# Optimization experiments

Measured on AMD Instinct MI355X. Metric: run time of the kernel, lower is better.

## Reference

```python
import jax, jax.numpy as jnp
import numpy as np

N_NODES = 100000
N_EDGES = 1600000
IN_CH = 128
HID = 128
OUT_CH = 64
N_GRAPHS = 512


def gcn_conv(x, edge_index, W, b):
    # GCNConv (PyG defaults): add self-loops, symmetric normalization
    # out = D^{-1/2} (A + I) D^{-1/2} X W + b
    n = x.shape[0]
    loop = jnp.arange(n, dtype=edge_index.dtype)
    src = jnp.concatenate([edge_index[0], loop])
    dst = jnp.concatenate([edge_index[1], loop])
    deg = jax.ops.segment_sum(jnp.ones_like(dst, x.dtype), dst, num_segments=n)
    dinv = jnp.where(deg > 0, jax.lax.rsqrt(deg), jnp.zeros_like(deg))
    norm = dinv[src] * dinv[dst]            # [E+N]
    h = x @ W                                # [N, out] transform first (dense GEMM)
    msg = h[src] * norm[:, None]             # gather + scale  [E+N, out]
    return jax.ops.segment_sum(msg, dst, num_segments=n) + b


def global_mean_pool(x, batch, num_graphs):
    sums = jax.ops.segment_sum(x, batch, num_segments=num_graphs)
    cnts = jax.ops.segment_sum(jnp.ones_like(batch, x.dtype), batch, num_segments=num_graphs)
    return sums / jnp.maximum(cnts, 1.0)[:, None]


def setup_inputs() -> dict:
    key = jax.random.key(0)
    ks = jax.random.split(key, 12)
    x = jax.random.normal(ks[0], (N_NODES, IN_CH), dtype=jnp.float32)
    edge_index = jax.random.randint(ks[1], (2, N_EDGES), 0, N_NODES, dtype=jnp.int64)
    batch = jnp.sort(jax.random.randint(ks[2], (N_NODES,), 0, N_GRAPHS, dtype=jnp.int64))
    def glorot(k, fi, fo):
        s = float(np.sqrt(6.0 / (fi + fo)))
        return jax.random.uniform(k, (fi, fo), jnp.float32, -s, s)
    W1 = glorot(ks[3], IN_CH, HID); b1 = jnp.zeros((HID,), jnp.float32)
    W2 = glorot(ks[4], HID, HID);   b2 = jnp.zeros((HID,), jnp.float32)
    W3 = glorot(ks[5], HID, HID);   b3 = jnp.zeros((HID,), jnp.float32)
    W4 = glorot(ks[6], HID, OUT_CH); b4 = jnp.zeros((OUT_CH,), jnp.float32)
    return {"x": x, "edge_index": edge_index, "batch": batch,
            "W1": W1, "b1": b1, "W2": W2, "b2": b2,
            "W3": W3, "b3": b3, "W4": W4, "b4": b4}


def reference(x, edge_index, batch, W1, b1, W2, b2, W3, b3, W4, b4):
    h = jax.nn.relu(gcn_conv(x, edge_index, W1, b1))
    h = jax.nn.relu(gcn_conv(h, edge_index, W2, b2))
    g = global_mean_pool(h, batch, N_GRAPHS)           # [G, HID]
    # MLP head; Dropout(0.2) is identity in eval mode
    g = jax.nn.relu(g @ W3 + b3)
    return g @ W4 + b4                                  # [G, OUT_CH]
```

## Files before the change

kernel.cpp:

```cpp
#include <hip/hip_runtime.h>

#define NN 100000
#define EE 1600000
#define CH 128
#define NG 512
#define OC 64

#define CSH 10
#define NCB 98
#define PBLK 256
#define PCHUNK 6250
#define SCAP 128

#define O_DINV   0
#define O_ROWS   100032
#define O_CNT    200064
#define O_PART   225152
#define O_OFFS   225280
#define O_START  225408
#define O_CSR    225984
#define O_HS     2726016
#define O_STG    9126080
#define O_WT1    9126080
#define O_WT2    9142464
#define O_A1     14800448

typedef __attribute__((ext_vector_type(8))) short short8v;
typedef __attribute__((ext_vector_type(4))) float float4v;

static __device__ __forceinline__ unsigned short f2bf(float x) {
  unsigned u = __float_as_uint(x);
  return (unsigned short)((u + 0x7FFFu + ((u >> 16) & 1u)) >> 16);
}
static __device__ __forceinline__ float bf2f(unsigned short h) {
  return __uint_as_float((unsigned)h << 16);
}
static __device__ __forceinline__ unsigned pack2(float a, float b) {
  return (unsigned)f2bf(a) | ((unsigned)f2bf(b) << 16);
}
static __device__ __forceinline__ float bflo(unsigned v) {
  return __uint_as_float(v << 16);
}
static __device__ __forceinline__ float bfhi(unsigned v) {
  return __uint_as_float(v & 0xFFFF0000u);
}

__global__ __launch_bounds__(1024) void k_part(const int* __restrict__ src,
                                               const int* __restrict__ dst,
                                               int* __restrict__ cnt,
                                               unsigned* __restrict__ stg) {
  __shared__ int hist[NCB];
  __shared__ int lcur[NCB];
  __shared__ unsigned lout[PCHUNK];
  int t = threadIdx.x;
  int e0 = blockIdx.x * PCHUNK;
  if (t < NCB) { hist[t] = 0; lcur[t] = 0; }
  __syncthreads();
  for (int e = e0 + t; e < e0 + PCHUNK; e += 1024)
    atomicAdd(&hist[dst[e] >> CSH], 1);
  __syncthreads();
  if (t == 0) {
    int s = 0;
    for (int i = 0; i < NCB; ++i) { int v = hist[i]; hist[i] = s; s += v; }
  }
  __syncthreads();
  for (int e = e0 + t; e < e0 + PCHUNK; e += 1024) {
    int d = dst[e];
    int b = d >> CSH;
    int p = hist[b] + atomicAdd(&lcur[b], 1);
    lout[p] = (unsigned)src[e] | ((unsigned)(d & 1023) << 17);
  }
  __syncthreads();
  int w = t >> 6, lane = t & 63;
  unsigned* mystg = stg + (size_t)blockIdx.x * NCB * SCAP;
  for (int b = w; b < NCB; b += 16) {
    int beg = hist[b];
    int end = (b == NCB - 1) ? PCHUNK : hist[b + 1];
    int n = min(end - beg, SCAP);
    for (int i = lane; i < n; i += 64) mystg[b * SCAP + i] = lout[beg + i];
    if (lane == 0) cnt[blockIdx.x * NCB + b] = n;
  }
}

__global__ __launch_bounds__(1024) void k_count(const unsigned* __restrict__ stg,
                                                const int* __restrict__ cnt,
                                                int* __restrict__ rows,
                                                int* __restrict__ part,
                                                float* __restrict__ dinv) {
  __shared__ int ldeg[1024];
  __shared__ int s[1024];
  int b = blockIdx.x;
  int t = threadIdx.x;
  int w = t >> 6, lane = t & 63;
  int gid = (b << CSH) + t;
  ldeg[t] = 0;
  __syncthreads();
  for (int blk = w; blk < PBLK; blk += 16) {
    int c = cnt[blk * NCB + b];
    const unsigned* p = stg + ((size_t)blk * NCB + b) * SCAP;
    for (int e = lane; e < c; e += 64) atomicAdd(&ldeg[p[e] >> 17], 1);
  }
  __syncthreads();
  int v = ldeg[t];
  if (gid < NN) dinv[gid] = rsqrtf((float)(v + 1));
  int pdeg = (v + 7) & ~7;
  s[t] = pdeg;
  __syncthreads();
  for (int off = 1; off < 1024; off <<= 1) {
    int u = (t >= off) ? s[t - off] : 0;
    __syncthreads();
    if (t >= off) s[t] += u;
    __syncthreads();
  }
  if (gid < NN) rows[gid] = s[t] - pdeg;
  if (t == 1023) part[b] = s[t];
}

__global__ void k_scan_part(const int* __restrict__ part, int* __restrict__ offs) {
  __shared__ int s[128];
  int t = threadIdx.x;
  int v = (t < NCB) ? part[t] : 0;
  s[t] = v;
  __syncthreads();
  for (int off = 1; off < 128; off <<= 1) {
    int u = (t >= off) ? s[t - off] : 0;
    __syncthreads();
    if (t >= off) s[t] += u;
    __syncthreads();
  }
  if (t < NCB) offs[t] = s[t] - v;
}

__global__ void k_scan_add(int* __restrict__ rows, const int* __restrict__ offs,
                           const int* __restrict__ part,
                           const int* __restrict__ batch, int* __restrict__ start) {
  int i = blockIdx.x * 256 + threadIdx.x;
  if (i >= NN) return;
  rows[i] += offs[i >> 10];
  if (i == 0) rows[NN] = offs[NCB - 1] + part[NCB - 1];
  int b = batch[i];
  int prev = (i == 0) ? -1 : batch[i - 1];
  for (int g = prev + 1; g <= b; ++g) start[g] = i;
  if (i == NN - 1)
    for (int g = b + 1; g <= NG; ++g) start[g] = NN;
}

__global__ __launch_bounds__(1024) void k_place(const unsigned* __restrict__ stg,
                                                const int* __restrict__ cnt,
                                                const int* __restrict__ rows,
                                                int* __restrict__ csr) {
  __shared__ int lrow[1024];
  __shared__ int lcur[1024];
  int b = blockIdx.x;
  int t = threadIdx.x;
  int w = t >> 6, lane = t & 63;
  int gid = (b << CSH) + t;
  lrow[t] = (gid < NN) ? rows[gid] : 0;
  lcur[t] = 0;
  __syncthreads();
  for (int blk = w; blk < PBLK; blk += 16) {
    int c = cnt[blk * NCB + b];
    const unsigned* p = stg + ((size_t)blk * NCB + b) * SCAP;
    for (int e = lane; e < c; e += 64) {
      unsigned x = p[e];
      int ld = x >> 17;
      int q = atomicAdd(&lcur[ld], 1);
      csr[lrow[ld] + q] = (int)(x & 0x1FFFFu);
    }
  }
  __syncthreads();
  int d = lcur[t];
  int pd = (d + 7) & ~7;
  int base = lrow[t];
  for (int i = d; i < pd; ++i) csr[base + i] = NN;
}

__global__ void k_wsplit(const float* __restrict__ W1, const float* __restrict__ W2,
                         unsigned short* __restrict__ wt1,
                         unsigned short* __restrict__ wt2) {
  int id = blockIdx.x * 256 + threadIdx.x;
  const float* W = (id < 16384) ? W1 : W2;
  unsigned short* wt = (id < 16384) ? wt1 : wt2;
  int i = id & 16383;
  int k = i >> 7, n = i & 127;
  float w = W[i];
  unsigned short h = f2bf(w);
  unsigned short l = f2bf(w - bf2f(h));
  wt[n * 128 + k] = h;
  wt[16384 + n * 128 + k] = l;
}

__global__ __launch_bounds__(256) void k_gemm_mfma(
    const float* __restrict__ X, const unsigned short* __restrict__ wth,
    const unsigned short* __restrict__ wtl, const float* __restrict__ dinv,
    unsigned short* __restrict__ Hs) {
  __shared__ __align__(16) unsigned short sWh[64 * 136];
  __shared__ __align__(16) unsigned short sWl[64 * 136];
  __shared__ __align__(16) unsigned short sXh[128 * 40];
  __shared__ __align__(16) unsigned short sXl[128 * 40];

  const int t = threadIdx.x;
  const int w = t >> 6, lane = t & 63;
  const int quad = lane >> 4, lr = lane & 15;
  const int row0 = blockIdx.x * 128;
  const int col0 = blockIdx.y * 64;

  if (blockIdx.x == 0 && blockIdx.y == 0 && t < 64)
    *(unsigned*)&Hs[(size_t)NN * CH + t * 2] = 0u;

#pragma unroll
  for (int j = 0; j < 8; ++j) {
    int id = t + j * 256;
    int n = id >> 5, kk = (id & 31) * 4;
    *(ushort4*)&sWh[n * 136 + kk] = *(const ushort4*)&wth[(col0 + n) * 128 + kk];
    *(ushort4*)&sWl[n * 136 + kk] = *(const ushort4*)&wtl[(col0 + n) * 128 + kk];
  }

  float4v acc[2][4];
#pragma unroll
  for (int mi = 0; mi < 2; ++mi)
#pragma unroll
    for (int ni = 0; ni < 4; ++ni) acc[mi][ni] = (float4v){0.f, 0.f, 0.f, 0.f};

  for (int ks = 0; ks < 4; ++ks) {
    const int k0 = ks * 32;
    if (ks) __syncthreads();
#pragma unroll
    for (int i = 0; i < 4; ++i) {
      int row = i * 32 + (t >> 3);
      int seg = t & 7;
      int gr = row0 + row;
      float4 xv = {0.f, 0.f, 0.f, 0.f};
      if (gr < NN) xv = *(const float4*)&X[(size_t)gr * CH + k0 + seg * 4];
      ushort4 h, l;
      h.x = f2bf(xv.x); l.x = f2bf(xv.x - bf2f(h.x));
      h.y = f2bf(xv.y); l.y = f2bf(xv.y - bf2f(h.y));
      h.z = f2bf(xv.z); l.z = f2bf(xv.z - bf2f(h.z));
      h.w = f2bf(xv.w); l.w = f2bf(xv.w - bf2f(h.w));
      *(ushort4*)&sXh[row * 40 + seg * 4] = h;
      *(ushort4*)&sXl[row * 40 + seg * 4] = l;
    }
    __syncthreads();

    short8v ah[2], al[2];
#pragma unroll
    for (int mi = 0; mi < 2; ++mi) {
      int r = w * 32 + mi * 16 + lr;
      ah[mi] = *(const short8v*)&sXh[r * 40 + quad * 8];
      al[mi] = *(const short8v*)&sXl[r * 40 + quad * 8];
    }
#pragma unroll
    for (int ni = 0; ni < 4; ++ni) {
      int n = ni * 16 + lr;
      short8v bh = *(const short8v*)&sWh[n * 136 + k0 + quad * 8];
      short8v bl = *(const short8v*)&sWl[n * 136 + k0 + quad * 8];
#pragma unroll
      for (int mi = 0; mi < 2; ++mi) {
        acc[mi][ni] = __builtin_amdgcn_mfma_f32_16x16x32_bf16(ah[mi], bh, acc[mi][ni], 0, 0, 0);
        acc[mi][ni] = __builtin_amdgcn_mfma_f32_16x16x32_bf16(ah[mi], bl, acc[mi][ni], 0, 0, 0);
        acc[mi][ni] = __builtin_amdgcn_mfma_f32_16x16x32_bf16(al[mi], bh, acc[mi][ni], 0, 0, 0);
      }
    }
  }

#pragma unroll
  for (int mi = 0; mi < 2; ++mi) {
#pragma unroll
    for (int r = 0; r < 4; ++r) {
      int grow = row0 + w * 32 + mi * 16 + quad * 4 + r;
      if (grow < NN) {
        float d = dinv[grow];
#pragma unroll
        for (int ni = 0; ni < 4; ++ni)
          Hs[(size_t)grow * CH + col0 + ni * 16 + lr] = f2bf(d * acc[mi][ni][r]);
      }
    }
  }
}

__global__ __launch_bounds__(256) void k_gemm_bf(
    const unsigned short* __restrict__ A, const unsigned short* __restrict__ wth,
    const unsigned short* __restrict__ wtl, const float* __restrict__ dinv,
    unsigned short* __restrict__ Hs) {
  __shared__ __align__(16) unsigned short sWh[64 * 136];
  __shared__ __align__(16) unsigned short sWl[64 * 136];
  __shared__ __align__(16) unsigned short sA[128 * 40];

  const int t = threadIdx.x;
  const int w = t >> 6, lane = t & 63;
  const int quad = lane >> 4, lr = lane & 15;
  const int row0 = blockIdx.x * 128;
  const int col0 = blockIdx.y * 64;

  if (blockIdx.x == 0 && blockIdx.y == 0 && t < 64)
    *(unsigned*)&Hs[(size_t)NN * CH + t * 2] = 0u;

#pragma unroll
  for (int j = 0; j < 8; ++j) {
    int id = t + j * 256;
    int n = id >> 5, kk = (id & 31) * 4;
    *(ushort4*)&sWh[n * 136 + kk] = *(const ushort4*)&wth[(col0 + n) * 128 + kk];
    *(ushort4*)&sWl[n * 136 + kk] = *(const ushort4*)&wtl[(col0 + n) * 128 + kk];
  }

  float4v acc[2][4];
#pragma unroll
  for (int mi = 0; mi < 2; ++mi)
#pragma unroll
    for (int ni = 0; ni < 4; ++ni) acc[mi][ni] = (float4v){0.f, 0.f, 0.f, 0.f};

  for (int ks = 0; ks < 4; ++ks) {
    const int k0 = ks * 32;
    if (ks) __syncthreads();
#pragma unroll
    for (int i = 0; i < 2; ++i) {
      int id = t + i * 256;
      int row = id >> 2, seg = id & 3;
      int gr = row0 + row;
      ushort4 v = {0, 0, 0, 0};
      if (gr < NN) v = *(const ushort4*)&A[(size_t)gr * CH + k0 + seg * 8];
      *(ushort4*)&sA[row * 40 + seg * 8] = v;
      ushort4 v2 = {0, 0, 0, 0};
      if (gr < NN) v2 = *(const ushort4*)&A[(size_t)gr * CH + k0 + seg * 8 + 4];
      *(ushort4*)&sA[row * 40 + seg * 8 + 4] = v2;
    }
    __syncthreads();

    short8v ah[2];
#pragma unroll
    for (int mi = 0; mi < 2; ++mi) {
      int r = w * 32 + mi * 16 + lr;
      ah[mi] = *(const short8v*)&sA[r * 40 + quad * 8];
    }
#pragma unroll
    for (int ni = 0; ni < 4; ++ni) {
      int n = ni * 16 + lr;
      short8v bh = *(const short8v*)&sWh[n * 136 + k0 + quad * 8];
      short8v bl = *(const short8v*)&sWl[n * 136 + k0 + quad * 8];
#pragma unroll
      for (int mi = 0; mi < 2; ++mi) {
        acc[mi][ni] = __builtin_amdgcn_mfma_f32_16x16x32_bf16(ah[mi], bh, acc[mi][ni], 0, 0, 0);
        acc[mi][ni] = __builtin_amdgcn_mfma_f32_16x16x32_bf16(ah[mi], bl, acc[mi][ni], 0, 0, 0);
      }
    }
  }

#pragma unroll
  for (int mi = 0; mi < 2; ++mi) {
#pragma unroll
    for (int r = 0; r < 4; ++r) {
      int grow = row0 + w * 32 + mi * 16 + quad * 4 + r;
      if (grow < NN) {
        float d = dinv[grow];
#pragma unroll
        for (int ni = 0; ni < 4; ++ni)
          Hs[(size_t)grow * CH + col0 + ni * 16 + lr] = f2bf(d * acc[mi][ni][r]);
      }
    }
  }
}

__global__ __launch_bounds__(256) void k_aggregate(
    const uint2* __restrict__ H2, const int* __restrict__ rows,
    const int* __restrict__ csr, const float* __restrict__ dinv,
    const float* __restrict__ bias, uint2* __restrict__ out) {
  int node = blockIdx.x * 4 + (threadIdx.x >> 6);
  if (node >= NN) return;
  int lane = threadIdx.x & 63;
  int h = lane >> 5, li = lane & 31;
  float a0 = 0.f, a1 = 0.f, a2 = 0.f, a3 = 0.f;
  int e0 = rows[node], e1 = rows[node + 1];
  int nr = (e1 - e0) >> 3;
  if (nr) {
    const int* cp = csr + e0 + h;
    uint2 va[4], vb[4];

#define LOADQ(buf)                                                          \
  do {                                                                      \
    unsigned s0_ = (unsigned)cp[0], s1_ = (unsigned)cp[2];                  \
    unsigned s2_ = (unsigned)cp[4], s3_ = (unsigned)cp[6];                  \
    buf[0] = H2[(s0_ << 5) | li];                                           \
    buf[1] = H2[(s1_ << 5) | li];                                           \
    buf[2] = H2[(s2_ << 5) | li];                                           \
    buf[3] = H2[(s3_ << 5) | li];                                           \
    cp += 8;                                                                \
  } while (0)

#define ACCQ(buf)                                                           \
  do {                                                                      \
    _Pragma("unroll")                                                       \
    for (int k_ = 0; k_ < 4; ++k_) {                                        \
      a0 += bflo(buf[k_].x); a1 += bfhi(buf[k_].x);                         \
      a2 += bflo(buf[k_].y); a3 += bfhi(buf[k_].y);                         \
    }                                                                       \
  } while (0)

    LOADQ(va);
    int rem = nr - 1;
    while (rem >= 2) {
      LOADQ(vb); ACCQ(va);
      LOADQ(va); ACCQ(vb);
      rem -= 2;
    }
    if (rem) { LOADQ(vb); ACCQ(va); ACCQ(vb); }
    else     { ACCQ(va); }
#undef LOADQ
#undef ACCQ
  }
  a0 += __shfl_xor(a0, 32);
  a1 += __shfl_xor(a1, 32);
  a2 += __shfl_xor(a2, 32);
  a3 += __shfl_xor(a3, 32);
  uint2 sv = H2[((unsigned)node << 5) | li];
  a0 += bflo(sv.x); a1 += bfhi(sv.x);
  a2 += bflo(sv.y); a3 += bfhi(sv.y);
  float d = dinv[node];
  float4 b4 = *(const float4*)&bias[li << 2];
  float o0 = fmaxf(fmaf(d, a0, b4.x), 0.f);
  float o1 = fmaxf(fmaf(d, a1, b4.y), 0.f);
  float o2 = fmaxf(fmaf(d, a2, b4.z), 0.f);
  float o3 = fmaxf(fmaf(d, a3, b4.w), 0.f);
  if (!h)
    out[((unsigned)node << 5) | li] = make_uint2(pack2(o0, o1), pack2(o2, o3));
}

__global__ __launch_bounds__(256) void k_head(
    const unsigned short* __restrict__ A, const int* __restrict__ start,
    const float* __restrict__ W3, const float* __restrict__ b3,
    const float* __restrict__ W4, const float* __restrict__ b4,
    float* __restrict__ out) {
  __shared__ float ppart[16][128];
  __shared__ float pooled[128];
  __shared__ float g1[128];
  int g = blockIdx.x;
  int t = threadIdx.x;
  int c8 = t & 15;
  int r = t >> 4;
  int s0 = start[g], s1 = start[g + 1];
  float s[8] = {0.f, 0.f, 0.f, 0.f, 0.f, 0.f, 0.f, 0.f};
  for (int i = s0 + r; i < s1; i += 16) {
    short8v v = *(const short8v*)&A[(size_t)i * CH + c8 * 8];
#pragma unroll
    for (int j = 0; j < 8; ++j) s[j] += bf2f((unsigned short)v[j]);
  }
#pragma unroll
  for (int j = 0; j < 8; ++j) ppart[r][c8 * 8 + j] = s[j];
  __syncthreads();
  if (t < 128) {
    float n = fmaxf((float)(s1 - s0), 1.0f);
    float acc = 0.f;
#pragma unroll
    for (int rr = 0; rr < 16; ++rr) acc += ppart[rr][t];
    pooled[t] = acc / n;
  }
  __syncthreads();
  if (t < 128) {
    float acc = b3[t];
    for (int k = 0; k < 128; ++k) acc += pooled[k] * W3[k * CH + t];
    g1[t] = fmaxf(acc, 0.f);
  }
  __syncthreads();
  if (t < 64) {
    float acc = b4[t];
    for (int k = 0; k < 128; ++k) acc += g1[k] * W4[k * OC + t];
    out[(size_t)g * OC + t] = acc;
  }
}

extern "C" void kernel_launch(void* const* d_in, const int* in_sizes, int n_in,
                              void* d_out, int out_size, void* d_ws, size_t ws_size,
                              hipStream_t stream) {
  const float* X   = (const float*)d_in[0];
  const int* ei    = (const int*)d_in[1];
  const int* batch = (const int*)d_in[2];
  const float* W1  = (const float*)d_in[3];
  const float* b1  = (const float*)d_in[4];
  const float* W2  = (const float*)d_in[5];
  const float* b2  = (const float*)d_in[6];
  const float* W3  = (const float*)d_in[7];
  const float* b3  = (const float*)d_in[8];
  const float* W4  = (const float*)d_in[9];
  const float* b4  = (const float*)d_in[10];
  float* out = (float*)d_out;
  float* ws = (float*)d_ws;

  const int* src = ei;
  const int* dst = ei + EE;

  float* dinv = ws + O_DINV;
  int* rows   = (int*)(ws + O_ROWS);
  int* cnt    = (int*)(ws + O_CNT);
  int* part   = (int*)(ws + O_PART);
  int* offs   = (int*)(ws + O_OFFS);
  int* start  = (int*)(ws + O_START);
  int* csr    = (int*)(ws + O_CSR);
  unsigned short* Hs = (unsigned short*)(ws + O_HS);
  unsigned* stg = (unsigned*)(ws + O_STG);
  unsigned short* wt1 = (unsigned short*)(ws + O_WT1);
  unsigned short* wt2 = (unsigned short*)(ws + O_WT2);
  unsigned short* A1 = (unsigned short*)(ws + O_A1);

  k_part<<<PBLK, 1024, 0, stream>>>(src, dst, cnt, stg);
  k_count<<<NCB, 1024, 0, stream>>>(stg, cnt, rows, part, dinv);
  k_scan_part<<<1, 128, 0, stream>>>(part, offs);
  k_scan_add<<<(NN + 255) / 256, 256, 0, stream>>>(rows, offs, part, batch, start);
  k_place<<<NCB, 1024, 0, stream>>>(stg, cnt, rows, csr);
  k_wsplit<<<128, 256, 0, stream>>>(W1, W2, wt1, wt2);

  dim3 ggrid((NN + 127) / 128, 2);
  k_gemm_mfma<<<ggrid, 256, 0, stream>>>(X, wt1, wt1 + 16384, dinv, Hs);
  k_aggregate<<<(NN + 3) / 4, 256, 0, stream>>>((const uint2*)Hs, rows, csr, dinv, b1, (uint2*)A1);
  k_gemm_bf<<<ggrid, 256, 0, stream>>>(A1, wt2, wt2 + 16384, dinv, Hs);
  k_aggregate<<<(NN + 3) / 4, 256, 0, stream>>>((const uint2*)Hs, rows, csr, dinv, b2, (uint2*)A1);

  k_head<<<NG, 256, 0, stream>>>(A1, start, W3, b3, W4, b4, out);
}
```

Measured before the change: 352.0 us.

## Split CSR count and place kernels across eight partition groups for more parallelism

The degree-count and CSR-placement kernels used to run only 98 blocks, each walking all 256 partition chunks. Each is now split into a 2D grid of 98x8 blocks, where every block handles 32 chunks and writes per-group degree slices. A new scan kernel sums those slices, and each placement block derives its base offset from the groups before it. Padding writes move into k_scan_add. This adds a kernel launch and extra global traffic for the per-group degree arrays in exchange for filling more compute units.

Measured after the change: 349.9 us. Within noise of the previous version (-0.6%).

```diff
diff --git a/kernel.cpp b/kernel.cpp
--- a/kernel.cpp
+++ b/kernel.cpp
@@ -11,6 +11,9 @@
 #define PBLK 256
 #define PCHUNK 6250
 #define SCAP 128
+#define NCG 8
+#define CPG 32
+#define DSL 100352
 
 #define O_DINV   0
 #define O_ROWS   100032
@@ -24,6 +27,8 @@
 #define O_WT1    9126080
 #define O_WT2    9142464
 #define O_A1     14800448
+#define O_DEG8   21200448
+#define O_DEG    22003264
 
 typedef __attribute__((ext_vector_type(8))) short short8v;
 typedef __attribute__((ext_vector_type(4))) float float4v;
@@ -82,27 +87,39 @@
   }
 }
 
-__global__ __launch_bounds__(1024) void k_count(const unsigned* __restrict__ stg,
-                                                const int* __restrict__ cnt,
+__global__ __launch_bounds__(1024) void k_count2(const unsigned* __restrict__ stg,
+                                                 const int* __restrict__ cnt,
+                                                 int* __restrict__ deg8) {
+  __shared__ int ldeg[1024];
+  int b = blockIdx.x, g = blockIdx.y;
+  int t = threadIdx.x;
+  int w = t >> 6, lane = t & 63;
+  ldeg[t] = 0;
+  __syncthreads();
+  for (int blk = g * CPG + w; blk < (g + 1) * CPG; blk += 16) {
+    int c = cnt[blk * NCB + b];
+    const unsigned* p = stg + ((size_t)blk * NCB + b) * SCAP;
+    for (int e = lane; e < c; e += 64) atomicAdd(&ldeg[p[e] >> 17], 1);
+  }
+  __syncthreads();
+  deg8[g * DSL + (b << CSH) + t] = ldeg[t];
+}
+
+__global__ __launch_bounds__(1024) void k_scan1(const int* __restrict__ deg8,
+                                                int* __restrict__ deg,
                                                 int* __restrict__ rows,
                                                 int* __restrict__ part,
                                                 float* __restrict__ dinv) {
-  __shared__ int ldeg[1024];
   __shared__ int s[1024];
-  int b = blockIdx.x;
-  int t = threadIdx.x;
-  int w = t >> 6, lane = t & 63;
+  int b = blockIdx.x, t = threadIdx.x;
   int gid = (b << CSH) + t;
-  ldeg[t] = 0;
-  __syncthreads();
-  for (int blk = w; blk < PBLK; blk += 16) {
-    int c = cnt[blk * NCB + b];
-    const unsigned* p = stg + ((size_t)blk * NCB + b) * SCAP;
-    for (int e = lane; e < c; e += 64) atomicAdd(&ldeg[p[e] >> 17], 1);
-  }
-  __syncthreads();
-  int v = ldeg[t];
-  if (gid < NN) dinv[gid] = rsqrtf((float)(v + 1));
+  int v = 0;
+#pragma unroll
+  for (int g = 0; g < NCG; ++g) v += deg8[g * DSL + gid];
+  if (gid < NN) {
+    dinv[gid] = rsqrtf((float)(v + 1));
+    deg[gid] = v;
+  }
   int pdeg = (v + 7) & ~7;
   s[t] = pdeg;
   __syncthreads();
@@ -132,12 +149,17 @@
 }
 
 __global__ void k_scan_add(int* __restrict__ rows, const int* __restrict__ offs,
-                           const int* __restrict__ part,
-                           const int* __restrict__ batch, int* __restrict__ start) {
+                           const int* __restrict__ part, const int* __restrict__ deg,
+                           const int* __restrict__ batch, int* __restrict__ start,
+                           int* __restrict__ csr) {
   int i = blockIdx.x * 256 + threadIdx.x;
   if (i >= NN) return;
-  rows[i] += offs[i >> 10];
+  int r = rows[i] + offs[i >> 10];
+  rows[i] = r;
   if (i == 0) rows[NN] = offs[NCB - 1] + part[NCB - 1];
+  int d = deg[i];
+  int pd = (d + 7) & ~7;
+  for (int k = r + d; k < r + pd; ++k) csr[k] = NN;
   int b = batch[i];
   int prev = (i == 0) ? -1 : batch[i - 1];
   for (int g = prev + 1; g <= b; ++g) start[g] = i;
@@ -145,20 +167,23 @@
     for (int g = b + 1; g <= NG; ++g) start[g] = NN;
 }
 
-__global__ __launch_bounds__(1024) void k_place(const unsigned* __restrict__ stg,
-                                                const int* __restrict__ cnt,
-                                                const int* __restrict__ rows,
-                                                int* __restrict__ csr) {
+__global__ __launch_bounds__(1024) void k_place2(const unsigned* __restrict__ stg,
+                                                 const int* __restrict__ cnt,
+                                                 const int* __restrict__ rows,
+                                                 const int* __restrict__ deg8,
+                                                 int* __restrict__ csr) {
   __shared__ int lrow[1024];
   __shared__ int lcur[1024];
-  int b = blockIdx.x;
+  int b = blockIdx.x, g = blockIdx.y;
   int t = threadIdx.x;
   int w = t >> 6, lane = t & 63;
   int gid = (b << CSH) + t;
-  lrow[t] = (gid < NN) ? rows[gid] : 0;
+  int base = (gid < NN) ? rows[gid] : 0;
+  for (int gp = 0; gp < g; ++gp) base += deg8[gp * DSL + gid];
+  lrow[t] = base;
   lcur[t] = 0;
   __syncthreads();
-  for (int blk = w; blk < PBLK; blk += 16) {
+  for (int blk = g * CPG + w; blk < (g + 1) * CPG; blk += 16) {
     int c = cnt[blk * NCB + b];
     const unsigned* p = stg + ((size_t)blk * NCB + b) * SCAP;
     for (int e = lane; e < c; e += 64) {
@@ -168,11 +193,6 @@
       csr[lrow[ld] + q] = (int)(x & 0x1FFFFu);
     }
   }
-  __syncthreads();
-  int d = lcur[t];
-  int pd = (d + 7) & ~7;
-  int base = lrow[t];
-  for (int i = d; i < pd; ++i) csr[base + i] = NN;
 }
 
 __global__ void k_wsplit(const float* __restrict__ W1, const float* __restrict__ W2,
@@ -499,12 +519,15 @@
   unsigned short* wt1 = (unsigned short*)(ws + O_WT1);
   unsigned short* wt2 = (unsigned short*)(ws + O_WT2);
   unsigned short* A1 = (unsigned short*)(ws + O_A1);
+  int* deg8   = (int*)(ws + O_DEG8);
+  int* deg    = (int*)(ws + O_DEG);
 
   k_part<<<PBLK, 1024, 0, stream>>>(src, dst, cnt, stg);
-  k_count<<<NCB, 1024, 0, stream>>>(stg, cnt, rows, part, dinv);
+  k_count2<<<dim3(NCB, NCG), 1024, 0, stream>>>(stg, cnt, deg8);
+  k_scan1<<<NCB, 1024, 0, stream>>>(deg8, deg, rows, part, dinv);
   k_scan_part<<<1, 128, 0, stream>>>(part, offs);
-  k_scan_add<<<(NN + 255) / 256, 256, 0, stream>>>(rows, offs, part, batch, start);
-  k_place<<<NCB, 1024, 0, stream>>>(stg, cnt, rows, csr);
+  k_scan_add<<<(NN + 255) / 256, 256, 0, stream>>>(rows, offs, part, deg, batch, start, csr);
+  k_place2<<<dim3(NCB, NCG), 1024, 0, stream>>>(stg, cnt, rows, deg8, csr);
   k_wsplit<<<128, 256, 0, stream>>>(W1, W2, wt1, wt2);
 
   dim3 ggrid((NN + 127) / 128, 2);
```
